# Kernel optimization log

Measured on AMD Instinct MI355X. Metric: run time of the kernel, lower is better.

Reference implementation:

```python
import jax, jax.numpy as jnp
import numpy as np

MUL0, MUL1 = 64, 32      # multiplicities of 0e scalars and 1o vectors
N = 200000               # number of nodes
EPS = 1e-8
LOG2 = float(np.log(2.0))


def setup_inputs() -> dict:
    key = jax.random.key(0)
    ks = jax.random.split(key, 9)
    f32 = jnp.float32
    return {
        "node_input": jax.random.normal(ks[0], (N, MUL0 + 3 * MUL1), f32),  # 64x0e + 32x1o
        "node_attr": jax.random.normal(ks[1], (N, 1), f32),                  # 1x0e
        "field": jax.random.normal(ks[2], (N, 3), f32),                      # 1x1o
        "W_tp_0e": jax.random.normal(ks[3], (MUL1, MUL0), f32),  # path 1o(x)1o->0e
        "W_tp_1o": jax.random.normal(ks[4], (MUL0, MUL1), f32),  # path 0e(x)1o->1o
        "W_lin_0e": jax.random.normal(ks[5], (MUL0, MUL0), f32),
        "W_lin_1o": jax.random.normal(ks[6], (MUL1, MUL1), f32),
        "W_sc_0e": jax.random.normal(ks[7], (MUL0, MUL0), f32),
        "W_sc_1o": jax.random.normal(ks[8], (MUL1, MUL1), f32),
    }


def _ssp(x):
    # shift_softplus
    return jax.nn.softplus(x) - LOG2


def reference(node_input, node_attr, field, W_tp_0e, W_tp_1o, W_lin_0e, W_lin_1o, W_sc_0e, W_sc_1o):
    x0 = node_input[:, :MUL0]                        # [N,64]  0e scalars
    x1 = node_input[:, MUL0:].reshape(-1, MUL1, 3)   # [N,32,3] 1o vectors

    # tp = FullyConnectedTensorProduct(input, 1x1o -> output)
    # e3nn 'component' irrep norm + 'element' path norm:
    # path 1o(x)1o->0e : w3j = I/sqrt(3), alpha = 1/mul1  -> coef 1/sqrt(3*mul1)
    t0 = (1.0 / np.sqrt(3.0 * MUL1)) * jnp.einsum('num,nm,uw->nw', x1, field, W_tp_0e)   # [N,64]
    # path 0e(x)1o->1o : w3j = I/sqrt(3), alpha = 3/mul0 -> coef 1/sqrt(mul0)
    t1 = (1.0 / np.sqrt(MUL0)) * jnp.einsum('nu,nm,uw->nwm', x0, field, W_tp_1o)         # [N,32,3]

    # lin2 = Linear(tp.irreps_out.simplify() -> output): per-irrep block linear, coef 1/sqrt(fan_in)
    y0 = (1.0 / np.sqrt(MUL0)) * (t0 @ W_lin_0e)                                          # [N,64]
    y1 = (1.0 / np.sqrt(MUL1)) * jnp.einsum('num,uw->nwm', t1, W_lin_1o)                  # [N,32,3]

    # sc = FCTP(features, 1x0e attr -> output): scalar-gated per-irrep linear, coef 1/sqrt(mul)
    a = node_attr[:, 0]
    z0 = (1.0 / np.sqrt(MUL0)) * jnp.einsum('nu,n,uw->nw', y0, a, W_sc_0e)
    z1 = (1.0 / np.sqrt(MUL1)) * jnp.einsum('num,n,uw->nwm', y1, a, W_sc_1o)

    # residual
    r0 = x0 + z0
    r1 = x1 + z1

    # NormActivation(shift_softplus, normalize=True, epsilon=1e-8, bias=False)
    n0 = jnp.sqrt(r0 * r0 + EPS * EPS)                          # [N,64]
    o0 = r0 * (_ssp(n0) / n0)
    n1 = jnp.sqrt(jnp.sum(r1 * r1, axis=-1) + EPS * EPS)        # [N,32]
    o1 = r1 * (_ssp(n1) / n1)[..., None]

    return jnp.concatenate([o0, o1.reshape(-1, 3 * MUL1)], axis=-1)   # [N,160]
```

## Files before the change

kernel.cpp:

```cpp
#include <hip/hip_runtime.h>
#include <math.h>

#define MUL0 64
#define MUL1 32
#define ROW_F 160
#define EPS2 1.0e-16f
#define LOG2F_ 0.69314718055994531f
#define LP 65
#define WPB 2
#define TPB (WPB * 64)

#define OT0   0
#define OL0   2048
#define OS0   6144
#define OT1   10240
#define OL1   12288
#define OS1   13312
#define OM0   14336
#define OM1   16384
#define CW_LDS 18432

__global__ __launch_bounds__(1024)
void combine_weights(const float* __restrict__ Wtp0,
                     const float* __restrict__ Wtp1,
                     const float* __restrict__ Wlin0,
                     const float* __restrict__ Wlin1,
                     const float* __restrict__ Wsc0,
                     const float* __restrict__ Wsc1,
                     float* __restrict__ ws)
{
    __shared__ float L[CW_LDS];
    const int t = threadIdx.x;

    {
        const float* srcs[6] = {Wtp0, Wlin0, Wsc0, Wtp1, Wlin1, Wsc1};
        const int    offs[6] = {OT0, OL0, OS0, OT1, OL1, OS1};
        const int    n4s[6]  = {512, 1024, 1024, 512, 256, 256};
#pragma unroll
        for (int m = 0; m < 6; ++m) {
            const float4* s = (const float4*)srcs[m];
            float4* d = (float4*)(L + offs[m]);
            for (int i = t; i < n4s[m]; i += 1024) d[i] = s[i];
        }
    }
    __syncthreads();

    if (t < 512) {
        const int u = t >> 4, q = t & 15;
        float4 acc = {0.f, 0.f, 0.f, 0.f};
#pragma unroll 8
        for (int k = 0; k < 64; ++k) {
            const float a = L[OT0 + u * 64 + k];
            const float4 b = ((const float4*)(L + OL0))[k * 16 + q];
            acc.x += a * b.x; acc.y += a * b.y; acc.z += a * b.z; acc.w += a * b.w;
        }
        ((float4*)(L + OM0))[u * 16 + q] = acc;
    } else {
        const int t2 = t - 512;
        const int u = t2 >> 3, q = t2 & 7;
        float4 acc = {0.f, 0.f, 0.f, 0.f};
#pragma unroll 8
        for (int k = 0; k < 32; ++k) {
            const float a = L[OT1 + u * 32 + k];
            const float4 b = ((const float4*)(L + OL1))[k * 8 + q];
            acc.x += a * b.x; acc.y += a * b.y; acc.z += a * b.z; acc.w += a * b.w;
        }
        ((float4*)(L + OM1))[u * 8 + q] = acc;
    }
    __syncthreads();

    const float C0 = 1.0f / (sqrtf(96.0f) * 64.0f);
    const float C1 = 1.0f / 256.0f;
    if (t < 512) {
        const int u = t >> 4, q = t & 15;
        float4 acc = {0.f, 0.f, 0.f, 0.f};
#pragma unroll 8
        for (int k = 0; k < 64; ++k) {
            const float a = L[OM0 + u * 64 + k];
            const float4 b = ((const float4*)(L + OS0))[k * 16 + q];
            acc.x += a * b.x; acc.y += a * b.y; acc.z += a * b.z; acc.w += a * b.w;
        }
        acc.x *= C0; acc.y *= C0; acc.z *= C0; acc.w *= C0;
        ((float4*)ws)[u * 16 + q] = acc;
    } else {
        const int t2 = t - 512;
        const int u = t2 >> 3, q = t2 & 7;
        float4 acc = {0.f, 0.f, 0.f, 0.f};
#pragma unroll 8
        for (int k = 0; k < 32; ++k) {
            const float a = L[OM1 + u * 32 + k];
            const float4 b = ((const float4*)(L + OS1))[k * 8 + q];
            acc.x += a * b.x; acc.y += a * b.y; acc.z += a * b.z; acc.w += a * b.w;
        }
        acc.x *= C1; acc.y *= C1; acc.z *= C1; acc.w *= C1;
        ((float4*)(ws + 2048))[u * 8 + q] = acc;
    }
}

__device__ __forceinline__ float ssp_over_n(float n)
{
    float sp = n + __logf(1.0f + __expf(-n)) - LOG2F_;
    return __fdividef(sp, n);
}

__device__ __forceinline__ void wave_fence()
{
    __asm__ volatile("" ::: "memory");
    __builtin_amdgcn_wave_barrier();
}

template<int W>
struct Stage {
    float4 v[W / 4];

    __device__ __forceinline__ void issue(const float* __restrict__ g,
                                          int lane, int rmax)
    {
        constexpr int NF4 = W / 4;
#pragma unroll
        for (int k = 0; k < NF4; ++k) {
            int id = k * 64 + lane;
            int r = id / NF4, gg = id % NF4;
            int rr = r <= rmax ? r : rmax;
            v[k] = *(const float4*)(g + rr * ROW_F + 4 * gg);
        }
    }

    __device__ __forceinline__ void commit(float* buf, int lane, float* dst)
    {
        constexpr int NF4 = W / 4;
        wave_fence();
#pragma unroll
        for (int k = 0; k < NF4; ++k) {
            int id = k * 64 + lane;
            int r = id / NF4, gg = id % NF4;
            buf[(4 * gg + 0) * LP + r] = v[k].x;
            buf[(4 * gg + 1) * LP + r] = v[k].y;
            buf[(4 * gg + 2) * LP + r] = v[k].z;
            buf[(4 * gg + 3) * LP + r] = v[k].w;
        }
        wave_fence();
#pragma unroll
        for (int c = 0; c < W; ++c) dst[c] = buf[c * LP + lane];
    }
};

template<int W>
__device__ __forceinline__ void stage_out(float* __restrict__ g, float* buf,
                                          int lane, int rmax, const float* src)
{
    constexpr int NF4 = W / 4;
    wave_fence();
#pragma unroll
    for (int c = 0; c < W; ++c) buf[c * LP + lane] = src[c];
    wave_fence();
#pragma unroll
    for (int k = 0; k < NF4; ++k) {
        int id = k * 64 + lane;
        int r = id / NF4, gg = id % NF4;
        int rr = r <= rmax ? r : rmax;
        float4 v;
        v.x = buf[(4 * gg + 0) * LP + r];
        v.y = buf[(4 * gg + 1) * LP + r];
        v.z = buf[(4 * gg + 2) * LP + r];
        v.w = buf[(4 * gg + 3) * LP + r];
        *(float4*)(g + rr * ROW_F + 4 * gg) = v;
    }
}

__global__ __launch_bounds__(TPB, 3)
void field_main(const float* __restrict__ in,
                const float* __restrict__ attr,
                const float* __restrict__ field,
                const float* __restrict__ Wg,
                float* __restrict__ out,
                int nrows)
{
    __shared__ float tbuf[WPB][48 * LP];

    const int tid = threadIdx.x;
    const int wv = tid >> 6, lane = tid & 63;
    int r0 = (blockIdx.x * WPB + wv) * 64;
    if (r0 > nrows - 64) r0 = nrows - 64;
    if (r0 < 0) r0 = 0;
    const int rmax = min(63, nrows - 1 - r0);
    const int rowe = r0 + min(lane, rmax);

    const float a  = attr[rowe];
    const float f0 = field[3 * rowe + 0];
    const float f1 = field[3 * rowe + 1];
    const float f2 = field[3 * rowe + 2];
    const float af0 = a * f0, af1 = a * f1, af2 = a * f2;

    const float* gin  = in  + (size_t)r0 * ROW_F;
    float*       gout = out + (size_t)r0 * ROW_F;
    float* buf = tbuf[wv];

    float x0r[64];
    {
        Stage<32> A, B;
        A.issue(gin,      lane, rmax);
        B.issue(gin + 32, lane, rmax);
        A.commit(buf, lane, x0r);
        B.commit(buf, lane, x0r + 32);
    }

    Stage<48> C;
    C.issue(gin + 64, lane, rmax);

    float pw[32];
#pragma unroll
    for (int w = 0; w < 32; ++w) pw[w] = 0.f;
#pragma unroll 4
    for (int u = 0; u < 64; ++u) {
        const float xu = x0r[u];
        const float4* wr = (const float4*)(Wg + 2048 + u * 32);
#pragma unroll
        for (int j = 0; j < 8; ++j) {
            float4 t = wr[j];
            pw[4 * j + 0] += xu * t.x;
            pw[4 * j + 1] += xu * t.y;
            pw[4 * j + 2] += xu * t.z;
            pw[4 * j + 3] += xu * t.w;
        }
    }
#pragma unroll
    for (int w = 0; w < 32; ++w) pw[w] *= a;

    float s1[32];
    Stage<48> D;

    {
        float c[48];
        C.commit(buf, lane, c);
#pragma unroll
        for (int i = 0; i < 16; ++i) {
            const int u = i;
            const float m0 = c[3 * i], m1 = c[3 * i + 1], m2 = c[3 * i + 2];
            s1[u] = m0 * af0 + m1 * af1 + m2 * af2;
            const float p = pw[u];
            float q0 = m0 + p * f0;
            float q1 = m1 + p * f1;
            float q2 = m2 + p * f2;
            float n = sqrtf(q0 * q0 + q1 * q1 + q2 * q2 + EPS2);
            float t = ssp_over_n(n);
            c[3 * i] = q0 * t; c[3 * i + 1] = q1 * t; c[3 * i + 2] = q2 * t;
        }
        wave_fence();
#pragma unroll
        for (int cc = 0; cc < 48; ++cc) buf[cc * LP + lane] = c[cc];
        D.issue(gin + 64 + 48, lane, rmax);
        wave_fence();
        float* g = gout + 64;
#pragma unroll
        for (int k = 0; k < 12; ++k) {
            int id = k * 64 + lane;
            int r = id / 12, gg = id % 12;
            int rr = r <= rmax ? r : rmax;
            float4 v;
            v.x = buf[(4 * gg + 0) * LP + r];
            v.y = buf[(4 * gg + 1) * LP + r];
            v.z = buf[(4 * gg + 2) * LP + r];
            v.w = buf[(4 * gg + 3) * LP + r];
            *(float4*)(g + rr * ROW_F + 4 * gg) = v;
        }
    }

    {
        float c[48];
        D.commit(buf, lane, c);
#pragma unroll
        for (int i = 0; i < 16; ++i) {
            const int u = 16 + i;
            const float m0 = c[3 * i], m1 = c[3 * i + 1], m2 = c[3 * i + 2];
            s1[u] = m0 * af0 + m1 * af1 + m2 * af2;
            const float p = pw[u];
            float q0 = m0 + p * f0;
            float q1 = m1 + p * f1;
            float q2 = m2 + p * f2;
            float n = sqrtf(q0 * q0 + q1 * q1 + q2 * q2 + EPS2);
            float t = ssp_over_n(n);
            c[3 * i] = q0 * t; c[3 * i + 1] = q1 * t; c[3 * i + 2] = q2 * t;
        }
        stage_out<48>(gout + 64 + 48, buf, lane, rmax, c);
    }

#pragma unroll
    for (int wc = 0; wc < 2; ++wc) {
        float acc[32];
#pragma unroll
        for (int j = 0; j < 32; ++j) acc[j] = 0.f;
#pragma unroll 4
        for (int u = 0; u < 32; ++u) {
            const float su = s1[u];
            const float4* wr = (const float4*)(Wg + u * 64 + 32 * wc);
#pragma unroll
            for (int j = 0; j < 8; ++j) {
                float4 t = wr[j];
                acc[4 * j + 0] += su * t.x;
                acc[4 * j + 1] += su * t.y;
                acc[4 * j + 2] += su * t.z;
                acc[4 * j + 3] += su * t.w;
            }
        }
#pragma unroll
        for (int j = 0; j < 32; ++j) {
            float r = x0r[32 * wc + j] + acc[j];
            float n = sqrtf(r * r + EPS2);
            acc[j] = r * ssp_over_n(n);
        }
        stage_out<32>(gout + 32 * wc, buf, lane, rmax, acc);
    }
}

extern "C" void kernel_launch(void* const* d_in, const int* in_sizes, int n_in,
                              void* d_out, int out_size, void* d_ws, size_t ws_size,
                              hipStream_t stream)
{
    const float* node_input = (const float*)d_in[0];
    const float* node_attr  = (const float*)d_in[1];
    const float* field      = (const float*)d_in[2];
    const float* Wtp0       = (const float*)d_in[3];
    const float* Wtp1       = (const float*)d_in[4];
    const float* Wlin0      = (const float*)d_in[5];
    const float* Wlin1      = (const float*)d_in[6];
    const float* Wsc0       = (const float*)d_in[7];
    const float* Wsc1       = (const float*)d_in[8];
    float* out = (float*)d_out;
    float* ws  = (float*)d_ws;

    const int nrows = in_sizes[0] / ROW_F;

    hipLaunchKernelGGL(combine_weights, dim3(1), dim3(1024), 0, stream,
                       Wtp0, Wtp1, Wlin0, Wlin1, Wsc0, Wsc1, ws);

    const int nwaves = (nrows + 63) / 64;
    const int nb = (nwaves + WPB - 1) / WPB;
    hipLaunchKernelGGL(field_main, dim3(nb), dim3(TPB), 0, stream,
                       node_input, node_attr, field, ws, out, nrows);
}
```

Before: 386.7 us.

## Drop LDS transpose staging; load and store rows directly per thread

Removes the shared-memory transpose staging, so each thread reads and writes its own 640-byte row with float4 accesses straight to global memory. The block shrinks to one wave of 64 threads and the weight loops are fully unrolled, with the 64-wide z0 accumulator kept in registers. This drops the LDS traffic and wave barriers, but accesses become strided across lanes rather than coalesced. Register pressure also rises (x0r, c0, c1 and z0a live together), which may cut occupancy.

New measurement: 461.7 us. 1.19x slower.

```diff
diff --git a/kernel.cpp b/kernel.cpp
--- a/kernel.cpp
+++ b/kernel.cpp
@@ -6,9 +6,6 @@
 #define ROW_F 160
 #define EPS2 1.0e-16f
 #define LOG2F_ 0.69314718055994531f
-#define LP 65
-#define WPB 2
-#define TPB (WPB * 64)
 
 #define OT0   0
 #define OL0   2048
@@ -103,72 +100,7 @@
     return __fdividef(sp, n);
 }
 
-__device__ __forceinline__ void wave_fence()
-{
-    __asm__ volatile("" ::: "memory");
-    __builtin_amdgcn_wave_barrier();
-}
-
-template<int W>
-struct Stage {
-    float4 v[W / 4];
-
-    __device__ __forceinline__ void issue(const float* __restrict__ g,
-                                          int lane, int rmax)
-    {
-        constexpr int NF4 = W / 4;
-#pragma unroll
-        for (int k = 0; k < NF4; ++k) {
-            int id = k * 64 + lane;
-            int r = id / NF4, gg = id % NF4;
-            int rr = r <= rmax ? r : rmax;
-            v[k] = *(const float4*)(g + rr * ROW_F + 4 * gg);
-        }
-    }
-
-    __device__ __forceinline__ void commit(float* buf, int lane, float* dst)
-    {
-        constexpr int NF4 = W / 4;
-        wave_fence();
-#pragma unroll
-        for (int k = 0; k < NF4; ++k) {
-            int id = k * 64 + lane;
-            int r = id / NF4, gg = id % NF4;
-            buf[(4 * gg + 0) * LP + r] = v[k].x;
-            buf[(4 * gg + 1) * LP + r] = v[k].y;
-            buf[(4 * gg + 2) * LP + r] = v[k].z;
-            buf[(4 * gg + 3) * LP + r] = v[k].w;
-        }
-        wave_fence();
-#pragma unroll
-        for (int c = 0; c < W; ++c) dst[c] = buf[c * LP + lane];
-    }
-};
-
-template<int W>
-__device__ __forceinline__ void stage_out(float* __restrict__ g, float* buf,
-                                          int lane, int rmax, const float* src)
-{
-    constexpr int NF4 = W / 4;
-    wave_fence();
-#pragma unroll
-    for (int c = 0; c < W; ++c) buf[c * LP + lane] = src[c];
-    wave_fence();
-#pragma unroll
-    for (int k = 0; k < NF4; ++k) {
-        int id = k * 64 + lane;
-        int r = id / NF4, gg = id % NF4;
-        int rr = r <= rmax ? r : rmax;
-        float4 v;
-        v.x = buf[(4 * gg + 0) * LP + r];
-        v.y = buf[(4 * gg + 1) * LP + r];
-        v.z = buf[(4 * gg + 2) * LP + r];
-        v.w = buf[(4 * gg + 3) * LP + r];
-        *(float4*)(g + rr * ROW_F + 4 * gg) = v;
-    }
-}
-
-__global__ __launch_bounds__(TPB, 3)
+__global__ __launch_bounds__(64)
 void field_main(const float* __restrict__ in,
                 const float* __restrict__ attr,
                 const float* __restrict__ field,
@@ -176,48 +108,36 @@
                 float* __restrict__ out,
                 int nrows)
 {
-    __shared__ float tbuf[WPB][48 * LP];
-
-    const int tid = threadIdx.x;
-    const int wv = tid >> 6, lane = tid & 63;
-    int r0 = (blockIdx.x * WPB + wv) * 64;
-    if (r0 > nrows - 64) r0 = nrows - 64;
-    if (r0 < 0) r0 = 0;
-    const int rmax = min(63, nrows - 1 - r0);
-    const int rowe = r0 + min(lane, rmax);
-
-    const float a  = attr[rowe];
-    const float f0 = field[3 * rowe + 0];
-    const float f1 = field[3 * rowe + 1];
-    const float f2 = field[3 * rowe + 2];
+    const int lane = threadIdx.x;
+    int row = blockIdx.x * 64 + lane;
+    if (row >= nrows) row = nrows - 1;
+    const float4* gin4  = (const float4*)(in  + (size_t)row * ROW_F);
+    float4*       gout4 = (float4*)(out + (size_t)row * ROW_F);
+
+    float x0r[64], c0[48], c1[48];
+#pragma unroll
+    for (int k = 0; k < 16; ++k) ((float4*)x0r)[k] = gin4[k];
+#pragma unroll
+    for (int k = 0; k < 12; ++k) ((float4*)c0)[k] = gin4[16 + k];
+#pragma unroll
+    for (int k = 0; k < 12; ++k) ((float4*)c1)[k] = gin4[28 + k];
+
+    const float a  = attr[row];
+    const float f0 = field[3 * row + 0];
+    const float f1 = field[3 * row + 1];
+    const float f2 = field[3 * row + 2];
     const float af0 = a * f0, af1 = a * f1, af2 = a * f2;
 
-    const float* gin  = in  + (size_t)r0 * ROW_F;
-    float*       gout = out + (size_t)r0 * ROW_F;
-    float* buf = tbuf[wv];
-
-    float x0r[64];
-    {
-        Stage<32> A, B;
-        A.issue(gin,      lane, rmax);
-        B.issue(gin + 32, lane, rmax);
-        A.commit(buf, lane, x0r);
-        B.commit(buf, lane, x0r + 32);
-    }
-
-    Stage<48> C;
-    C.issue(gin + 64, lane, rmax);
-
     float pw[32];
 #pragma unroll
     for (int w = 0; w < 32; ++w) pw[w] = 0.f;
-#pragma unroll 4
+#pragma unroll
     for (int u = 0; u < 64; ++u) {
         const float xu = x0r[u];
         const float4* wr = (const float4*)(Wg + 2048 + u * 32);
 #pragma unroll
         for (int j = 0; j < 8; ++j) {
-            float4 t = wr[j];
+            const float4 t = wr[j];
             pw[4 * j + 0] += xu * t.x;
             pw[4 * j + 1] += xu * t.y;
             pw[4 * j + 2] += xu * t.z;
@@ -228,89 +148,61 @@
     for (int w = 0; w < 32; ++w) pw[w] *= a;
 
     float s1[32];
-    Stage<48> D;
-
-    {
-        float c[48];
-        C.commit(buf, lane, c);
-#pragma unroll
-        for (int i = 0; i < 16; ++i) {
-            const int u = i;
-            const float m0 = c[3 * i], m1 = c[3 * i + 1], m2 = c[3 * i + 2];
-            s1[u] = m0 * af0 + m1 * af1 + m2 * af2;
-            const float p = pw[u];
-            float q0 = m0 + p * f0;
-            float q1 = m1 + p * f1;
-            float q2 = m2 + p * f2;
-            float n = sqrtf(q0 * q0 + q1 * q1 + q2 * q2 + EPS2);
-            float t = ssp_over_n(n);
-            c[3 * i] = q0 * t; c[3 * i + 1] = q1 * t; c[3 * i + 2] = q2 * t;
-        }
-        wave_fence();
-#pragma unroll
-        for (int cc = 0; cc < 48; ++cc) buf[cc * LP + lane] = c[cc];
-        D.issue(gin + 64 + 48, lane, rmax);
-        wave_fence();
-        float* g = gout + 64;
-#pragma unroll
-        for (int k = 0; k < 12; ++k) {
-            int id = k * 64 + lane;
-            int r = id / 12, gg = id % 12;
-            int rr = r <= rmax ? r : rmax;
-            float4 v;
-            v.x = buf[(4 * gg + 0) * LP + r];
-            v.y = buf[(4 * gg + 1) * LP + r];
-            v.z = buf[(4 * gg + 2) * LP + r];
-            v.w = buf[(4 * gg + 3) * LP + r];
-            *(float4*)(g + rr * ROW_F + 4 * gg) = v;
-        }
-    }
-
-    {
-        float c[48];
-        D.commit(buf, lane, c);
-#pragma unroll
-        for (int i = 0; i < 16; ++i) {
-            const int u = 16 + i;
-            const float m0 = c[3 * i], m1 = c[3 * i + 1], m2 = c[3 * i + 2];
-            s1[u] = m0 * af0 + m1 * af1 + m2 * af2;
-            const float p = pw[u];
-            float q0 = m0 + p * f0;
-            float q1 = m1 + p * f1;
-            float q2 = m2 + p * f2;
-            float n = sqrtf(q0 * q0 + q1 * q1 + q2 * q2 + EPS2);
-            float t = ssp_over_n(n);
-            c[3 * i] = q0 * t; c[3 * i + 1] = q1 * t; c[3 * i + 2] = q2 * t;
-        }
-        stage_out<48>(gout + 64 + 48, buf, lane, rmax, c);
-    }
-
-#pragma unroll
-    for (int wc = 0; wc < 2; ++wc) {
-        float acc[32];
-#pragma unroll
-        for (int j = 0; j < 32; ++j) acc[j] = 0.f;
-#pragma unroll 4
-        for (int u = 0; u < 32; ++u) {
-            const float su = s1[u];
-            const float4* wr = (const float4*)(Wg + u * 64 + 32 * wc);
-#pragma unroll
-            for (int j = 0; j < 8; ++j) {
-                float4 t = wr[j];
-                acc[4 * j + 0] += su * t.x;
-                acc[4 * j + 1] += su * t.y;
-                acc[4 * j + 2] += su * t.z;
-                acc[4 * j + 3] += su * t.w;
-            }
-        }
-#pragma unroll
-        for (int j = 0; j < 32; ++j) {
-            float r = x0r[32 * wc + j] + acc[j];
-            float n = sqrtf(r * r + EPS2);
-            acc[j] = r * ssp_over_n(n);
-        }
-        stage_out<32>(gout + 32 * wc, buf, lane, rmax, acc);
-    }
+
+#pragma unroll
+    for (int i = 0; i < 16; ++i) {
+        const float m0 = c0[3 * i], m1 = c0[3 * i + 1], m2 = c0[3 * i + 2];
+        s1[i] = m0 * af0 + m1 * af1 + m2 * af2;
+        const float p = pw[i];
+        float q0 = m0 + p * f0;
+        float q1 = m1 + p * f1;
+        float q2 = m2 + p * f2;
+        float n = sqrtf(q0 * q0 + q1 * q1 + q2 * q2 + EPS2);
+        float t = ssp_over_n(n);
+        c0[3 * i] = q0 * t; c0[3 * i + 1] = q1 * t; c0[3 * i + 2] = q2 * t;
+    }
+#pragma unroll
+    for (int k = 0; k < 12; ++k) gout4[16 + k] = ((float4*)c0)[k];
+
+#pragma unroll
+    for (int i = 0; i < 16; ++i) {
+        const float m0 = c1[3 * i], m1 = c1[3 * i + 1], m2 = c1[3 * i + 2];
+        s1[16 + i] = m0 * af0 + m1 * af1 + m2 * af2;
+        const float p = pw[16 + i];
+        float q0 = m0 + p * f0;
+        float q1 = m1 + p * f1;
+        float q2 = m2 + p * f2;
+        float n = sqrtf(q0 * q0 + q1 * q1 + q2 * q2 + EPS2);
+        float t = ssp_over_n(n);
+        c1[3 * i] = q0 * t; c1[3 * i + 1] = q1 * t; c1[3 * i + 2] = q2 * t;
+    }
+#pragma unroll
+    for (int k = 0; k < 12; ++k) gout4[28 + k] = ((float4*)c1)[k];
+
+    float z0a[64];
+#pragma unroll
+    for (int w = 0; w < 64; ++w) z0a[w] = 0.f;
+#pragma unroll
+    for (int u = 0; u < 32; ++u) {
+        const float su = s1[u];
+        const float4* wr = (const float4*)(Wg + u * 64);
+#pragma unroll
+        for (int j = 0; j < 16; ++j) {
+            const float4 t = wr[j];
+            z0a[4 * j + 0] += su * t.x;
+            z0a[4 * j + 1] += su * t.y;
+            z0a[4 * j + 2] += su * t.z;
+            z0a[4 * j + 3] += su * t.w;
+        }
+    }
+#pragma unroll
+    for (int w = 0; w < 64; ++w) {
+        const float r = x0r[w] + z0a[w];
+        const float n = sqrtf(r * r + EPS2);
+        z0a[w] = r * ssp_over_n(n);
+    }
+#pragma unroll
+    for (int k = 0; k < 16; ++k) gout4[k] = ((float4*)z0a)[k];
 }
 
 extern "C" void kernel_launch(void* const* d_in, const int* in_sizes, int n_in,
@@ -334,8 +226,7 @@
     hipLaunchKernelGGL(combine_weights, dim3(1), dim3(1024), 0, stream,
                        Wtp0, Wtp1, Wlin0, Wlin1, Wsc0, Wsc1, ws);
 
-    const int nwaves = (nrows + 63) / 64;
-    const int nb = (nwaves + WPB - 1) / WPB;
-    hipLaunchKernelGGL(field_main, dim3(nb), dim3(TPB), 0, stream,
+    const int nb = (nrows + 63) / 64;
+    hipLaunchKernelGGL(field_main, dim3(nb), dim3(64), 0, stream,
                        node_input, node_attr, field, ws, out, nrows);
 }
```

## Keep transposed tiles in LDS and re-read x0 from global to cut registers

Applied to the files above, without the earlier changes.

The kernel no longer keeps the 64-wide x0 row block and intermediate tiles in registers. Values are read straight from the LDS transpose buffer, x0 is reloaded from global memory for the residual instead of being held live, and all input loads are issued up front. The last linear is merged into a single pass producing both 32-column halves. This lowers register pressure to allow more occupancy or deeper latency hiding, at the cost of extra LDS traffic, a second global read of x0, and more live float4 staging registers early in the kernel.

Measured after the change: 349.7 us. 1.11x faster.

```diff
diff --git a/kernel.cpp b/kernel.cpp
--- a/kernel.cpp
+++ b/kernel.cpp
@@ -126,7 +126,7 @@
         }
     }
 
-    __device__ __forceinline__ void commit(float* buf, int lane, float* dst)
+    __device__ __forceinline__ void commitL(float* buf, int lane)
     {
         constexpr int NF4 = W / 4;
         wave_fence();
@@ -140,31 +140,26 @@
             buf[(4 * gg + 3) * LP + r] = v[k].w;
         }
         wave_fence();
-#pragma unroll
-        for (int c = 0; c < W; ++c) dst[c] = buf[c * LP + lane];
     }
 };
 
 template<int W>
-__device__ __forceinline__ void stage_out(float* __restrict__ g, float* buf,
-                                          int lane, int rmax, const float* src)
+__device__ __forceinline__ void flushL(float* __restrict__ g, const float* buf,
+                                       int lane, int rmax)
 {
     constexpr int NF4 = W / 4;
-    wave_fence();
-#pragma unroll
-    for (int c = 0; c < W; ++c) buf[c * LP + lane] = src[c];
     wave_fence();
 #pragma unroll
     for (int k = 0; k < NF4; ++k) {
         int id = k * 64 + lane;
         int r = id / NF4, gg = id % NF4;
         int rr = r <= rmax ? r : rmax;
-        float4 v;
-        v.x = buf[(4 * gg + 0) * LP + r];
-        v.y = buf[(4 * gg + 1) * LP + r];
-        v.z = buf[(4 * gg + 2) * LP + r];
-        v.w = buf[(4 * gg + 3) * LP + r];
-        *(float4*)(g + rr * ROW_F + 4 * gg) = v;
+        float4 o;
+        o.x = buf[(4 * gg + 0) * LP + r];
+        o.y = buf[(4 * gg + 1) * LP + r];
+        o.z = buf[(4 * gg + 2) * LP + r];
+        o.w = buf[(4 * gg + 3) * LP + r];
+        *(float4*)(g + rr * ROW_F + 4 * gg) = o;
     }
 }
 
@@ -196,121 +191,140 @@
     float*       gout = out + (size_t)r0 * ROW_F;
     float* buf = tbuf[wv];
 
-    float x0r[64];
-    {
-        Stage<32> A, B;
-        A.issue(gin,      lane, rmax);
-        B.issue(gin + 32, lane, rmax);
-        A.commit(buf, lane, x0r);
-        B.commit(buf, lane, x0r + 32);
-    }
-
-    Stage<48> C;
-    C.issue(gin + 64, lane, rmax);
+    Stage<32> XA, XB;
+    Stage<48> C0;
+    XA.issue(gin,      lane, rmax);
+    XB.issue(gin + 32, lane, rmax);
+    C0.issue(gin + 64, lane, rmax);
 
     float pw[32];
 #pragma unroll
     for (int w = 0; w < 32; ++w) pw[w] = 0.f;
-#pragma unroll 4
-    for (int u = 0; u < 64; ++u) {
-        const float xu = x0r[u];
+
+    XA.commitL(buf, lane);
+#pragma unroll 2
+    for (int u = 0; u < 32; ++u) {
+        const float xu = buf[u * LP + lane];
         const float4* wr = (const float4*)(Wg + 2048 + u * 32);
 #pragma unroll
         for (int j = 0; j < 8; ++j) {
-            float4 t = wr[j];
+            const float4 t = wr[j];
             pw[4 * j + 0] += xu * t.x;
             pw[4 * j + 1] += xu * t.y;
             pw[4 * j + 2] += xu * t.z;
             pw[4 * j + 3] += xu * t.w;
         }
     }
+    XB.commitL(buf, lane);
+#pragma unroll 2
+    for (int u = 0; u < 32; ++u) {
+        const float xu = buf[u * LP + lane];
+        const float4* wr = (const float4*)(Wg + 3072 + u * 32);
+#pragma unroll
+        for (int j = 0; j < 8; ++j) {
+            const float4 t = wr[j];
+            pw[4 * j + 0] += xu * t.x;
+            pw[4 * j + 1] += xu * t.y;
+            pw[4 * j + 2] += xu * t.z;
+            pw[4 * j + 3] += xu * t.w;
+        }
+    }
 #pragma unroll
     for (int w = 0; w < 32; ++w) pw[w] *= a;
 
     float s1[32];
-    Stage<48> D;
-
-    {
-        float c[48];
-        C.commit(buf, lane, c);
-#pragma unroll
-        for (int i = 0; i < 16; ++i) {
-            const int u = i;
-            const float m0 = c[3 * i], m1 = c[3 * i + 1], m2 = c[3 * i + 2];
-            s1[u] = m0 * af0 + m1 * af1 + m2 * af2;
-            const float p = pw[u];
-            float q0 = m0 + p * f0;
-            float q1 = m1 + p * f1;
-            float q2 = m2 + p * f2;
-            float n = sqrtf(q0 * q0 + q1 * q1 + q2 * q2 + EPS2);
-            float t = ssp_over_n(n);
-            c[3 * i] = q0 * t; c[3 * i + 1] = q1 * t; c[3 * i + 2] = q2 * t;
-        }
-        wave_fence();
-#pragma unroll
-        for (int cc = 0; cc < 48; ++cc) buf[cc * LP + lane] = c[cc];
-        D.issue(gin + 64 + 48, lane, rmax);
-        wave_fence();
-        float* g = gout + 64;
-#pragma unroll
-        for (int k = 0; k < 12; ++k) {
-            int id = k * 64 + lane;
-            int r = id / 12, gg = id % 12;
-            int rr = r <= rmax ? r : rmax;
-            float4 v;
-            v.x = buf[(4 * gg + 0) * LP + r];
-            v.y = buf[(4 * gg + 1) * LP + r];
-            v.z = buf[(4 * gg + 2) * LP + r];
-            v.w = buf[(4 * gg + 3) * LP + r];
-            *(float4*)(g + rr * ROW_F + 4 * gg) = v;
-        }
-    }
-
-    {
-        float c[48];
-        D.commit(buf, lane, c);
-#pragma unroll
-        for (int i = 0; i < 16; ++i) {
-            const int u = 16 + i;
-            const float m0 = c[3 * i], m1 = c[3 * i + 1], m2 = c[3 * i + 2];
-            s1[u] = m0 * af0 + m1 * af1 + m2 * af2;
-            const float p = pw[u];
-            float q0 = m0 + p * f0;
-            float q1 = m1 + p * f1;
-            float q2 = m2 + p * f2;
-            float n = sqrtf(q0 * q0 + q1 * q1 + q2 * q2 + EPS2);
-            float t = ssp_over_n(n);
-            c[3 * i] = q0 * t; c[3 * i + 1] = q1 * t; c[3 * i + 2] = q2 * t;
-        }
-        stage_out<48>(gout + 64 + 48, buf, lane, rmax, c);
-    }
-
-#pragma unroll
-    for (int wc = 0; wc < 2; ++wc) {
-        float acc[32];
-#pragma unroll
-        for (int j = 0; j < 32; ++j) acc[j] = 0.f;
-#pragma unroll 4
-        for (int u = 0; u < 32; ++u) {
-            const float su = s1[u];
-            const float4* wr = (const float4*)(Wg + u * 64 + 32 * wc);
-#pragma unroll
-            for (int j = 0; j < 8; ++j) {
-                float4 t = wr[j];
-                acc[4 * j + 0] += su * t.x;
-                acc[4 * j + 1] += su * t.y;
-                acc[4 * j + 2] += su * t.z;
-                acc[4 * j + 3] += su * t.w;
-            }
-        }
-#pragma unroll
-        for (int j = 0; j < 32; ++j) {
-            float r = x0r[32 * wc + j] + acc[j];
-            float n = sqrtf(r * r + EPS2);
-            acc[j] = r * ssp_over_n(n);
-        }
-        stage_out<32>(gout + 32 * wc, buf, lane, rmax, acc);
-    }
+    Stage<48> C1;
+
+    C0.commitL(buf, lane);
+    C1.issue(gin + 64 + 48, lane, rmax);
+#pragma unroll
+    for (int i = 0; i < 16; ++i) {
+        const float m0 = buf[(3 * i + 0) * LP + lane];
+        const float m1 = buf[(3 * i + 1) * LP + lane];
+        const float m2 = buf[(3 * i + 2) * LP + lane];
+        s1[i] = m0 * af0 + m1 * af1 + m2 * af2;
+        const float p = pw[i];
+        float q0 = m0 + p * f0;
+        float q1 = m1 + p * f1;
+        float q2 = m2 + p * f2;
+        float n = sqrtf(q0 * q0 + q1 * q1 + q2 * q2 + EPS2);
+        float t = ssp_over_n(n);
+        buf[(3 * i + 0) * LP + lane] = q0 * t;
+        buf[(3 * i + 1) * LP + lane] = q1 * t;
+        buf[(3 * i + 2) * LP + lane] = q2 * t;
+    }
+    flushL<48>(gout + 64, buf, lane, rmax);
+
+    C1.commitL(buf, lane);
+#pragma unroll
+    for (int i = 0; i < 16; ++i) {
+        const float m0 = buf[(3 * i + 0) * LP + lane];
+        const float m1 = buf[(3 * i + 1) * LP + lane];
+        const float m2 = buf[(3 * i + 2) * LP + lane];
+        s1[16 + i] = m0 * af0 + m1 * af1 + m2 * af2;
+        const float p = pw[16 + i];
+        float q0 = m0 + p * f0;
+        float q1 = m1 + p * f1;
+        float q2 = m2 + p * f2;
+        float n = sqrtf(q0 * q0 + q1 * q1 + q2 * q2 + EPS2);
+        float t = ssp_over_n(n);
+        buf[(3 * i + 0) * LP + lane] = q0 * t;
+        buf[(3 * i + 1) * LP + lane] = q1 * t;
+        buf[(3 * i + 2) * LP + lane] = q2 * t;
+    }
+    flushL<48>(gout + 64 + 48, buf, lane, rmax);
+
+    wave_fence();
+#pragma unroll
+    for (int i = 0; i < 32; ++i) buf[i * LP + lane] = s1[i];
+    wave_fence();
+
+    Stage<32> XR0, XR1;
+    XR0.issue(gin,      lane, rmax);
+    XR1.issue(gin + 32, lane, rmax);
+
+    float acc0[32], acc1[32];
+#pragma unroll
+    for (int j = 0; j < 32; ++j) { acc0[j] = 0.f; acc1[j] = 0.f; }
+#pragma unroll 2
+    for (int u = 0; u < 32; ++u) {
+        const float su = buf[u * LP + lane];
+        const float4* wr = (const float4*)(Wg + u * 64);
+#pragma unroll
+        for (int j = 0; j < 8; ++j) {
+            const float4 t = wr[j];
+            acc0[4 * j + 0] += su * t.x;
+            acc0[4 * j + 1] += su * t.y;
+            acc0[4 * j + 2] += su * t.z;
+            acc0[4 * j + 3] += su * t.w;
+        }
+#pragma unroll
+        for (int j = 0; j < 8; ++j) {
+            const float4 t = wr[8 + j];
+            acc1[4 * j + 0] += su * t.x;
+            acc1[4 * j + 1] += su * t.y;
+            acc1[4 * j + 2] += su * t.z;
+            acc1[4 * j + 3] += su * t.w;
+        }
+    }
+
+    XR0.commitL(buf, lane);
+#pragma unroll
+    for (int j = 0; j < 32; ++j) {
+        const float r = buf[j * LP + lane] + acc0[j];
+        const float n = sqrtf(r * r + EPS2);
+        buf[j * LP + lane] = r * ssp_over_n(n);
+    }
+    flushL<32>(gout, buf, lane, rmax);
+
+    XR1.commitL(buf, lane);
+#pragma unroll
+    for (int j = 0; j < 32; ++j) {
+        const float r = buf[j * LP + lane] + acc1[j];
+        const float n = sqrtf(r * r + EPS2);
+        buf[j * LP + lane] = r * ssp_over_n(n);
+    }
+    flushL<32>(gout + 32, buf, lane, rmax);
 }
 
 extern "C" void kernel_launch(void* const* d_in, const int* in_sizes, int n_in,
```
